# Kernel optimization log

Hardware: AMD Instinct MI355X
Metric: run time of the kernel (lower is better)

The kernel has to match this reference:

```python
import jax, jax.numpy as jnp
import numpy as np
import math

TWO_PI = 2.0 * math.pi
LN_EPS = 1e-5


def _phase(pos_f, d):
    # periods[i, j] = i * d + j + 2 ; phi[s, i, j] = cos(2*pi*k_s / periods[i, j])
    i = jnp.arange(d, dtype=jnp.float32)
    periods = i[:, None] * d + i[None, :] + 2.0  # (d, d)
    return jnp.cos(TWO_PI * pos_f[:, None, None] / periods)  # (S, d, d)


def _layernorm(x, g, b):
    mu = jnp.mean(x, axis=-1, keepdims=True)
    var = jnp.mean(jnp.square(x - mu), axis=-1, keepdims=True)
    return (x - mu) * jax.lax.rsqrt(var + LN_EPS) * g + b


def _pos_nk(x, P, phi):
    # Nk[b, s, i] = sum_j P[i, j] * x[b, s, j] * phi[s, i, j]
    return jnp.einsum('bsj,ij,sij->bsi', x, P, phi)


def setup_inputs() -> dict:
    key = jax.random.key(0)
    ks = jax.random.split(key, 10)
    B, S, V, D = 4, 4096, 64, 128
    NTOK = 64  # 4^3 k-mer tokens
    u = lambda k, shp, a: jax.random.uniform(k, shp, jnp.float32, -a, a)
    return {
        'tokens': jax.random.randint(ks[0], (B, S), 0, NTOK, dtype=jnp.int32),
        'positions': jnp.arange(S, dtype=jnp.int32),
        'emb': jax.random.normal(ks[1], (NTOK, V), jnp.float32),
        'char_P': u(ks[2], (V, V), 0.1),
        'M1': u(ks[3], (D, V), 0.5),
        'P1': u(ks[4], (D, D), 0.1),
        'g1': jnp.ones((D,), jnp.float32),
        'b1': jnp.zeros((D,), jnp.float32),
        'R1': u(ks[5], (D, V), 0.1),
        'M2': u(ks[6], (D, D), 0.5),
        'P2': u(ks[7], (D, D), 0.1),
        'g2': jnp.ones((D,), jnp.float32),
        'b2': jnp.zeros((D,), jnp.float32),
    }


def reference(tokens, positions, emb, char_P, M1, P1, g1, b1, R1, M2, P2, g2, b2):
    pos_f = positions.astype(jnp.float32)
    V, D1, D2 = emb.shape[1], M1.shape[0], M2.shape[0]
    # char level (Layer 0): embedding + position-modulated mixing
    x = emb[tokens]                               # (B, S, V)
    h = _pos_nk(x, char_P, _phase(pos_f, V))      # (B, S, V)
    # Layer 1: separate residual (in_dim != out_dim -> linear proj)
    t1 = jnp.einsum('bsj,ij->bsi', h, M1)         # (B, S, D1)
    n1 = _pos_nk(_layernorm(t1, g1, b1), P1, _phase(pos_f, D1))
    h1 = n1 + jnp.einsum('bsj,ij->bsi', h, R1)
    # Layer 2: shared residual (residual = x @ M.T, pre-norm)
    t2 = jnp.einsum('bsj,ij->bsi', h1, M2)        # (B, S, D2)
    n2 = _pos_nk(_layernorm(t2, g2, b2), P2, _phase(pos_f, D2))
    return n2 + t2
```

## Files before the change

kernel.cpp:

```cpp
#include <hip/hip_runtime.h>

typedef unsigned short u16;
typedef unsigned int   u32;
typedef float f32x2 __attribute__((ext_vector_type(2)));

#define BB 4
#define SS 4096
#define VV 64
#define DD 128

#define CPT_OFF 0
#define M1T_OFF 4096
#define R1T_OFF 12288
#define P1T_OFF 20480
#define M2T_OFF 36864
#define P2T_OFF 53248
#define EMB_OFF 69632
#define G1_OFF  73728
#define B1_OFF  73856
#define G2_OFF  73984
#define B2_OFF  74112
#define WS_F32_WEIGHTS 74240

__device__ __forceinline__ float bf2f(u16 u) {
    return __uint_as_float(((u32)u) << 16);
}
__device__ __forceinline__ float ldany(const void* p, int idx, bool f32) {
    return f32 ? ((const float*)p)[idx] : bf2f(((const u16*)p)[idx]);
}
__device__ __forceinline__ float phase_cos(float pos, float pf) {
    float x = pos * __builtin_amdgcn_rcpf(pf);
    float r = __builtin_amdgcn_fractf(x);
    return __builtin_amdgcn_cosf(r);
}
__device__ __forceinline__ float f4get(float4 v, int i) {
    return i == 0 ? v.x : i == 1 ? v.y : i == 2 ? v.z : v.w;
}
struct acc2x2 {
    f32x2 lo, hi;
    __device__ __forceinline__ void zero() { lo = (f32x2)0.f; hi = (f32x2)0.f; }
    __device__ __forceinline__ void fma(float s, float4 v) {
        f32x2 s2 = {s, s};
        f32x2 vlo = {v.x, v.y}, vhi = {v.z, v.w};
        lo = __builtin_elementwise_fma(s2, vlo, lo);
        hi = __builtin_elementwise_fma(s2, vhi, hi);
    }
    __device__ __forceinline__ float get(int b) const {
        return b == 0 ? lo[0] : b == 1 ? lo[1] : b == 2 ? hi[0] : hi[1];
    }
    __device__ __forceinline__ void red_xor(int m) {
        lo[0] += __shfl_xor(lo[0], m, 64);
        lo[1] += __shfl_xor(lo[1], m, 64);
        hi[0] += __shfl_xor(hi[0], m, 64);
        hi[1] += __shfl_xor(hi[1], m, 64);
    }
};

__global__ void prep_ws(const void* __restrict__ cP,  const void* __restrict__ M1,
                        const void* __restrict__ R1,  const void* __restrict__ P1,
                        const void* __restrict__ M2,  const void* __restrict__ P2,
                        const void* __restrict__ emb, const void* __restrict__ g1,
                        const void* __restrict__ b1,  const void* __restrict__ g2,
                        const void* __restrict__ b2,  float* __restrict__ wsf)
{
    const bool f32 = (((const u32*)g1)[0] == 0x3F800000u);
    const int m = blockIdx.x;
    const int t = threadIdx.x;
    if (m == 17) {
        for (int idx = t; idx < 4608; idx += 256) {
            float v; int dst;
            if (idx < 4096) { v = ldany(emb, idx, f32); dst = EMB_OFF + idx; }
            else {
                int off = idx - 4096, which = off >> 7, e = off & 127;
                const void* p = (which == 0) ? g1 : (which == 1) ? b1
                              : (which == 2) ? g2 : b2;
                v = ldany(p, e, f32);
                dst = G1_OFF + which * 128 + e;
            }
            wsf[dst] = v;
        }
        return;
    }
    __shared__ float tile[64][65];
    const void* src; int doff, R, C, ti0, tj0;
    if (m == 0)      { src = cP; doff = CPT_OFF; R = 64;  C = 64;  ti0 = 0;            tj0 = 0; }
    else if (m <= 2) { src = M1; doff = M1T_OFF; R = 128; C = 64;  ti0 = (m - 1) * 64; tj0 = 0; }
    else if (m <= 4) { src = R1; doff = R1T_OFF; R = 128; C = 64;  ti0 = (m - 3) * 64; tj0 = 0; }
    else {
        const int k = m - 5, w = k >> 2, q = k & 3;
        src  = (w == 0) ? P1 : (w == 1) ? M2 : P2;
        doff = (w == 0) ? P1T_OFF : (w == 1) ? M2T_OFF : P2T_OFF;
        R = 128; C = 128; ti0 = (q >> 1) * 64; tj0 = (q & 1) * 64;
    }
    float* dst = wsf + doff;
    #pragma unroll
    for (int k = 0; k < 16; ++k) {
        int idx = k * 256 + t;
        int i = idx >> 6, j = idx & 63;
        tile[i][j] = ldany(src, (ti0 + i) * C + (tj0 + j), f32);
    }
    __syncthreads();
    #pragma unroll
    for (int k = 0; k < 16; ++k) {
        int idx = k * 256 + t;
        int j = idx >> 6, i = idx & 63;
        int gj = tj0 + j, gi = ti0 + i;
        dst[((gj >> 2) * R + gi) * 4 + (gj & 3)] = tile[i][j];
    }
}

template<bool WS>
__global__ void __launch_bounds__(256, 3)
fused_hier(const int* __restrict__ tokens,
           const int* __restrict__ positions,
           const void* __restrict__ emb,
           const void* __restrict__ cP,
           const void* __restrict__ M1,
           const void* __restrict__ P1,
           const void* __restrict__ g1,
           const void* __restrict__ b1,
           const void* __restrict__ R1,
           const void* __restrict__ M2,
           const void* __restrict__ P2,
           const void* __restrict__ g2,
           const void* __restrict__ b2,
           const float* __restrict__ wsf,
           float* __restrict__ out)
{
    __shared__ float4 x4v[67];
    __shared__ float4 h4v[VV];
    __shared__ float4 lnv[131];
    __shared__ float4 h1v[131];
    __shared__ float  t14p[4 * DD];
    __shared__ float  t2p[4 * DD];
    __shared__ float  resp[4 * DD];

    float* x4  = (float*)x4v;
    float* h4  = (float*)h4v;
    float* lnf = (float*)lnv;
    float* h1f = (float*)h1v;

    const int t = threadIdx.x;
    const int s = blockIdx.x;
    if (s >= SS) return;
    const bool f32 = WS ? true : (((const u32*)g1)[0] == 0x3F800000u);
    const float pos = (float)positions[s];
    const int wv = t >> 6, L = t & 63;
    const int rp = wv * 16 + (L & 15);
    const int jq = (L >> 4) & 3;
    const int i7 = wv * 32 + (L & 31);
    const int jh = L >> 5;
    const int w  = wv, l = L;

    {
        int tok = tokens[wv * SS + s];
        int ie  = t & 63;
        float v = WS ? wsf[EMB_OFF + tok * VV + ie] : ldany(emb, tok * VV + ie, f32);
        x4[(ie + (ie >> 4)) * 4 + wv] = v;
    }
    __syncthreads();

    {
        acc2x2 a; a.zero();
        const int jb = jq * 16;
        float pf = (float)(rp * VV + jb + 2);
        #pragma unroll
        for (int q = 0; q < 4; ++q) {
            const int jg = jq * 4 + q;
            float4 w4;
            if (WS) w4 = *(const float4*)&wsf[CPT_OFF + (jg * VV + rp) * 4];
            #pragma unroll
            for (int k = 0; k < 4; ++k) {
                const int j = jb + q * 4 + k;
                float c  = phase_cos(pos, pf);
                float wt = (WS ? f4get(w4, k) : ldany(cP, rp * VV + j, f32)) * c;
                a.fma(wt, x4v[j + (j >> 4)]);
                pf += 1.0f;
            }
        }
        a.red_xor(16);
        a.red_xor(32);
        h4[rp * 4 + jq] = a.get(jq);
    }
    __syncthreads();

    {
        acc2x2 at, ar; at.zero(); ar.zero();
        #pragma unroll
        for (int q = 0; q < 8; ++q) {
            const int jg = jh * 8 + q;
            float4 m4, r4;
            if (WS) {
                m4 = *(const float4*)&wsf[M1T_OFF + (jg * DD + i7) * 4];
                r4 = *(const float4*)&wsf[R1T_OFF + (jg * DD + i7) * 4];
            }
            #pragma unroll
            for (int k = 0; k < 4; ++k) {
                const int j = jh * 32 + q * 4 + k;
                float mv = WS ? f4get(m4, k) : ldany(M1, i7 * VV + j, f32);
                float rv = WS ? f4get(r4, k) : ldany(R1, i7 * VV + j, f32);
                float4 hb = h4v[j];
                at.fma(mv, hb);
                ar.fma(rv, hb);
            }
        }
        at.red_xor(32);
        ar.red_xor(32);
        const int b0 = jh * 2, b1 = b0 + 1;
        t14p[b0 * 128 + i7] = at.get(b0);
        t14p[b1 * 128 + i7] = at.get(b1);
        resp[b0 * 128 + i7] = ar.get(b0);
        resp[b1 * 128 + i7] = ar.get(b1);
    }
    __syncthreads();

    {
        float v0 = t14p[w * 128 + l], v1 = t14p[w * 128 + 64 + l];
        float s1 = v0 + v1;
        #pragma unroll
        for (int m = 1; m < 64; m <<= 1) s1 += __shfl_xor(s1, m, 64);
        float mu = s1 * (1.0f / 128.0f);
        float d0 = v0 - mu, d1 = v1 - mu;
        float s2 = d0 * d0 + d1 * d1;
        #pragma unroll
        for (int m = 1; m < 64; m <<= 1) s2 += __shfl_xor(s2, m, 64);
        float rs = rsqrtf(s2 * (1.0f / 128.0f) + 1e-5f);
        float ga = WS ? wsf[G1_OFF + l]      : ldany(g1, l, f32);
        float gb = WS ? wsf[G1_OFF + l + 64] : ldany(g1, l + 64, f32);
        float ba = WS ? wsf[B1_OFF + l]      : ldany(b1, l, f32);
        float bb = WS ? wsf[B1_OFF + l + 64] : ldany(b1, l + 64, f32);
        const int pA = l + (l >> 5);
        const int pB = l + 66 + (l >> 5);
        lnf[pA * 4 + w] = d0 * rs * ga + ba;
        lnf[pB * 4 + w] = d1 * rs * gb + bb;
    }
    __syncthreads();

    {
        acc2x2 alo, ahi; alo.zero(); ahi.zero();
        const int jb = jq * 32;
        float pfa = (float)(rp * DD + jb + 2);
        float pfb = pfa + 8192.0f;
        #pragma unroll
        for (int q = 0; q < 8; ++q) {
            const int jg = jq * 8 + q;
            float4 wa, wb;
            if (WS) {
                wa = *(const float4*)&wsf[P1T_OFF + (jg * DD + rp) * 4];
                wb = *(const float4*)&wsf[P1T_OFF + (jg * DD + rp + 64) * 4];
            }
            #pragma unroll
            for (int k = 0; k < 4; ++k) {
                const int j = jb + q * 4 + k;
                float ca = phase_cos(pos, pfa);
                float cb = phase_cos(pos, pfb);
                float4 lnj = lnv[j + (j >> 5)];
                float wva = WS ? f4get(wa, k) : ldany(P1, rp * DD + j, f32);
                float wvb = WS ? f4get(wb, k) : ldany(P1, (rp + 64) * DD + j, f32);
                alo.fma(wva * ca, lnj);
                ahi.fma(wvb * cb, lnj);
                pfa += 1.0f; pfb += 1.0f;
            }
        }
        alo.red_xor(16); alo.red_xor(32);
        ahi.red_xor(16); ahi.red_xor(32);
        float r0 = resp[jq * 128 + rp];
        float r1 = resp[jq * 128 + rp + 64];
        h1f[(rp + (rp >> 5)) * 4 + jq]      = r0 + alo.get(jq);
        h1f[(rp + 66 + (rp >> 5)) * 4 + jq] = r1 + ahi.get(jq);
    }
    __syncthreads();

    float t2v0, t2v1;
    {
        acc2x2 alo, ahi; alo.zero(); ahi.zero();
        const int jb = jq * 32;
        #pragma unroll
        for (int q = 0; q < 8; ++q) {
            const int jg = jq * 8 + q;
            float4 wa, wb;
            if (WS) {
                wa = *(const float4*)&wsf[M2T_OFF + (jg * DD + rp) * 4];
                wb = *(const float4*)&wsf[M2T_OFF + (jg * DD + rp + 64) * 4];
            }
            #pragma unroll
            for (int k = 0; k < 4; ++k) {
                const int j = jb + q * 4 + k;
                float4 hj = h1v[j + (j >> 5)];
                float wva = WS ? f4get(wa, k) : ldany(M2, rp * DD + j, f32);
                float wvb = WS ? f4get(wb, k) : ldany(M2, (rp + 64) * DD + j, f32);
                alo.fma(wva, hj);
                ahi.fma(wvb, hj);
            }
        }
        alo.red_xor(16); alo.red_xor(32);
        ahi.red_xor(16); ahi.red_xor(32);
        t2v0 = alo.get(jq);
        t2v1 = ahi.get(jq);
        t2p[jq * 128 + rp]      = t2v0;
        t2p[jq * 128 + rp + 64] = t2v1;
    }
    __syncthreads();

    {
        float v0 = t2p[w * 128 + l], v1 = t2p[w * 128 + 64 + l];
        float s1 = v0 + v1;
        #pragma unroll
        for (int m = 1; m < 64; m <<= 1) s1 += __shfl_xor(s1, m, 64);
        float mu = s1 * (1.0f / 128.0f);
        float d0 = v0 - mu, d1 = v1 - mu;
        float s2 = d0 * d0 + d1 * d1;
        #pragma unroll
        for (int m = 1; m < 64; m <<= 1) s2 += __shfl_xor(s2, m, 64);
        float rs = rsqrtf(s2 * (1.0f / 128.0f) + 1e-5f);
        float ga = WS ? wsf[G2_OFF + l]      : ldany(g2, l, f32);
        float gb = WS ? wsf[G2_OFF + l + 64] : ldany(g2, l + 64, f32);
        float ba = WS ? wsf[B2_OFF + l]      : ldany(b2, l, f32);
        float bb = WS ? wsf[B2_OFF + l + 64] : ldany(b2, l + 64, f32);
        const int pA = l + (l >> 5);
        const int pB = l + 66 + (l >> 5);
        lnf[pA * 4 + w] = d0 * rs * ga + ba;
        lnf[pB * 4 + w] = d1 * rs * gb + bb;
    }
    __syncthreads();

    {
        acc2x2 alo, ahi; alo.zero(); ahi.zero();
        const int jb = jq * 32;
        float pfa = (float)(rp * DD + jb + 2);
        float pfb = pfa + 8192.0f;
        #pragma unroll
        for (int q = 0; q < 8; ++q) {
            const int jg = jq * 8 + q;
            float4 wa, wb;
            if (WS) {
                wa = *(const float4*)&wsf[P2T_OFF + (jg * DD + rp) * 4];
                wb = *(const float4*)&wsf[P2T_OFF + (jg * DD + rp + 64) * 4];
            }
            #pragma unroll
            for (int k = 0; k < 4; ++k) {
                const int j = jb + q * 4 + k;
                float ca = phase_cos(pos, pfa);
                float cb = phase_cos(pos, pfb);
                float4 lnj = lnv[j + (j >> 5)];
                float wva = WS ? f4get(wa, k) : ldany(P2, rp * DD + j, f32);
                float wvb = WS ? f4get(wb, k) : ldany(P2, (rp + 64) * DD + j, f32);
                alo.fma(wva * ca, lnj);
                ahi.fma(wvb * cb, lnj);
                pfa += 1.0f; pfb += 1.0f;
            }
        }
        alo.red_xor(16); alo.red_xor(32);
        ahi.red_xor(16); ahi.red_xor(32);
        out[(jq * SS + s) * DD + rp]      = alo.get(jq) + t2v0;
        out[(jq * SS + s) * DD + rp + 64] = ahi.get(jq) + t2v1;
    }
}

extern "C" void kernel_launch(void* const* d_in, const int* in_sizes, int n_in,
                              void* d_out, int out_size, void* d_ws, size_t ws_size,
                              hipStream_t stream)
{
    const int* tokens    = (const int*)d_in[0];
    const int* positions = (const int*)d_in[1];
    const void* emb = d_in[2];
    const void* cP  = d_in[3];
    const void* M1  = d_in[4];
    const void* P1  = d_in[5];
    const void* g1  = d_in[6];
    const void* b1  = d_in[7];
    const void* R1  = d_in[8];
    const void* M2  = d_in[9];
    const void* P2  = d_in[10];
    const void* g2  = d_in[11];
    const void* b2  = d_in[12];
    float* out = (float*)d_out;
    float* wsf = (float*)d_ws;

    const bool tw = (ws_size >= (size_t)WS_F32_WEIGHTS * sizeof(float));
    if (tw) {
        prep_ws<<<18, 256, 0, stream>>>(cP, M1, R1, P1, M2, P2, emb,
                                        g1, b1, g2, b2, wsf);
        fused_hier<true><<<SS, 256, 0, stream>>>(tokens, positions, emb, cP, M1, P1,
                                                 g1, b1, R1, M2, P2, g2, b2, wsf, out);
    } else {
        fused_hier<false><<<SS, 256, 0, stream>>>(tokens, positions, emb, cP, M1, P1,
                                                  g1, b1, R1, M2, P2, g2, b2, wsf, out);
    }
}
```

Before: 154.7 us.

## Use one wavefront per position with full reductions per lane

Each position's block shrinks from four wavefronts to one 64-lane wavefront. Every lane now owns whole output rows and runs the full reduction dimension itself, which removes the cross-lane shuffle reductions after each matvec. Each lane also computes all four batch LayerNorms in one pass. The trade-off is four times the serial work per thread, including the cosine phase evaluations, and fewer threads per block, so the kernel depends on many concurrent blocks to hide latency.

Measured after the change: 164.7 us. 1.06x slower.

```diff
diff --git a/kernel.cpp b/kernel.cpp
--- a/kernel.cpp
+++ b/kernel.cpp
@@ -22,6 +22,8 @@
 #define B2_OFF  74112
 #define WS_F32_WEIGHTS 74240
 
+#define SK(j) ((j) + ((j) >> 3))
+
 __device__ __forceinline__ float bf2f(u16 u) {
     return __uint_as_float(((u32)u) << 16);
 }
@@ -48,11 +50,8 @@
     __device__ __forceinline__ float get(int b) const {
         return b == 0 ? lo[0] : b == 1 ? lo[1] : b == 2 ? hi[0] : hi[1];
     }
-    __device__ __forceinline__ void red_xor(int m) {
-        lo[0] += __shfl_xor(lo[0], m, 64);
-        lo[1] += __shfl_xor(lo[1], m, 64);
-        hi[0] += __shfl_xor(hi[0], m, 64);
-        hi[1] += __shfl_xor(hi[1], m, 64);
+    __device__ __forceinline__ float4 as4() const {
+        return make_float4(lo[0], lo[1], hi[0], hi[1]);
     }
 };
 
@@ -110,7 +109,7 @@
 }
 
 template<bool WS>
-__global__ void __launch_bounds__(256, 3)
+__global__ void __launch_bounds__(64, 3)
 fused_hier(const int* __restrict__ tokens,
            const int* __restrict__ positions,
            const void* __restrict__ emb,
@@ -127,233 +126,259 @@
            const float* __restrict__ wsf,
            float* __restrict__ out)
 {
-    __shared__ float4 x4v[67];
-    __shared__ float4 h4v[VV];
-    __shared__ float4 lnv[131];
-    __shared__ float4 h1v[131];
-    __shared__ float  t14p[4 * DD];
-    __shared__ float  t2p[4 * DD];
-    __shared__ float  resp[4 * DD];
-
-    float* x4  = (float*)x4v;
-    float* h4  = (float*)h4v;
-    float* lnf = (float*)lnv;
-    float* h1f = (float*)h1v;
-
-    const int t = threadIdx.x;
+    __shared__ float4 x4v[72];
+    __shared__ float4 h4v[72];
+    __shared__ float4 lnv[144];
+    __shared__ float4 h1v[144];
+    __shared__ float  t14p[512];
+    __shared__ float  t2p[512];
+
+    const int l = threadIdx.x;
     const int s = blockIdx.x;
     if (s >= SS) return;
     const bool f32 = WS ? true : (((const u32*)g1)[0] == 0x3F800000u);
     const float pos = (float)positions[s];
-    const int wv = t >> 6, L = t & 63;
-    const int rp = wv * 16 + (L & 15);
-    const int jq = (L >> 4) & 3;
-    const int i7 = wv * 32 + (L & 31);
-    const int jh = L >> 5;
-    const int w  = wv, l = L;
-
-    {
-        int tok = tokens[wv * SS + s];
-        int ie  = t & 63;
-        float v = WS ? wsf[EMB_OFF + tok * VV + ie] : ldany(emb, tok * VV + ie, f32);
-        x4[(ie + (ie >> 4)) * 4 + wv] = v;
+
+    {
+        int tk0 = tokens[0 * SS + s], tk1 = tokens[1 * SS + s];
+        int tk2 = tokens[2 * SS + s], tk3 = tokens[3 * SS + s];
+        float4 xb;
+        xb.x = WS ? wsf[EMB_OFF + tk0 * VV + l] : ldany(emb, tk0 * VV + l, f32);
+        xb.y = WS ? wsf[EMB_OFF + tk1 * VV + l] : ldany(emb, tk1 * VV + l, f32);
+        xb.z = WS ? wsf[EMB_OFF + tk2 * VV + l] : ldany(emb, tk2 * VV + l, f32);
+        xb.w = WS ? wsf[EMB_OFF + tk3 * VV + l] : ldany(emb, tk3 * VV + l, f32);
+        x4v[SK(l)] = xb;
     }
     __syncthreads();
 
     {
         acc2x2 a; a.zero();
-        const int jb = jq * 16;
-        float pf = (float)(rp * VV + jb + 2);
-        #pragma unroll
-        for (int q = 0; q < 4; ++q) {
-            const int jg = jq * 4 + q;
+        float pf = (float)(l * VV + 2);
+        #pragma unroll
+        for (int q = 0; q < 16; ++q) {
             float4 w4;
-            if (WS) w4 = *(const float4*)&wsf[CPT_OFF + (jg * VV + rp) * 4];
+            if (WS) w4 = *(const float4*)&wsf[CPT_OFF + (q * VV + l) * 4];
             #pragma unroll
             for (int k = 0; k < 4; ++k) {
-                const int j = jb + q * 4 + k;
+                const int j = q * 4 + k;
                 float c  = phase_cos(pos, pf);
-                float wt = (WS ? f4get(w4, k) : ldany(cP, rp * VV + j, f32)) * c;
-                a.fma(wt, x4v[j + (j >> 4)]);
+                float wt = (WS ? f4get(w4, k) : ldany(cP, l * VV + j, f32)) * c;
+                a.fma(wt, x4v[SK(j)]);
                 pf += 1.0f;
             }
         }
-        a.red_xor(16);
-        a.red_xor(32);
-        h4[rp * 4 + jq] = a.get(jq);
-    }
-    __syncthreads();
-
-    {
-        acc2x2 at, ar; at.zero(); ar.zero();
-        #pragma unroll
-        for (int q = 0; q < 8; ++q) {
-            const int jg = jh * 8 + q;
-            float4 m4, r4;
+        h4v[SK(l)] = a.as4();
+    }
+    __syncthreads();
+
+    float4 res0, res1;
+    {
+        acc2x2 at0, at1, ar0, ar1;
+        at0.zero(); at1.zero(); ar0.zero(); ar1.zero();
+        #pragma unroll 8
+        for (int q = 0; q < 16; ++q) {
+            float4 ma, mb, ra, rb;
             if (WS) {
-                m4 = *(const float4*)&wsf[M1T_OFF + (jg * DD + i7) * 4];
-                r4 = *(const float4*)&wsf[R1T_OFF + (jg * DD + i7) * 4];
+                ma = *(const float4*)&wsf[M1T_OFF + (q * DD + l) * 4];
+                mb = *(const float4*)&wsf[M1T_OFF + (q * DD + l + 64) * 4];
+                ra = *(const float4*)&wsf[R1T_OFF + (q * DD + l) * 4];
+                rb = *(const float4*)&wsf[R1T_OFF + (q * DD + l + 64) * 4];
             }
             #pragma unroll
             for (int k = 0; k < 4; ++k) {
-                const int j = jh * 32 + q * 4 + k;
-                float mv = WS ? f4get(m4, k) : ldany(M1, i7 * VV + j, f32);
-                float rv = WS ? f4get(r4, k) : ldany(R1, i7 * VV + j, f32);
-                float4 hb = h4v[j];
-                at.fma(mv, hb);
-                ar.fma(rv, hb);
-            }
-        }
-        at.red_xor(32);
-        ar.red_xor(32);
-        const int b0 = jh * 2, b1 = b0 + 1;
-        t14p[b0 * 128 + i7] = at.get(b0);
-        t14p[b1 * 128 + i7] = at.get(b1);
-        resp[b0 * 128 + i7] = ar.get(b0);
-        resp[b1 * 128 + i7] = ar.get(b1);
-    }
-    __syncthreads();
-
-    {
-        float v0 = t14p[w * 128 + l], v1 = t14p[w * 128 + 64 + l];
-        float s1 = v0 + v1;
-        #pragma unroll
-        for (int m = 1; m < 64; m <<= 1) s1 += __shfl_xor(s1, m, 64);
-        float mu = s1 * (1.0f / 128.0f);
-        float d0 = v0 - mu, d1 = v1 - mu;
-        float s2 = d0 * d0 + d1 * d1;
-        #pragma unroll
-        for (int m = 1; m < 64; m <<= 1) s2 += __shfl_xor(s2, m, 64);
-        float rs = rsqrtf(s2 * (1.0f / 128.0f) + 1e-5f);
+                const int j = q * 4 + k;
+                float4 hb = h4v[SK(j)];
+                float m0 = WS ? f4get(ma, k) : ldany(M1, l * VV + j, f32);
+                float m1 = WS ? f4get(mb, k) : ldany(M1, (l + 64) * VV + j, f32);
+                float r0 = WS ? f4get(ra, k) : ldany(R1, l * VV + j, f32);
+                float r1 = WS ? f4get(rb, k) : ldany(R1, (l + 64) * VV + j, f32);
+                at0.fma(m0, hb); at1.fma(m1, hb);
+                ar0.fma(r0, hb); ar1.fma(r1, hb);
+            }
+        }
+        #pragma unroll
+        for (int b = 0; b < 4; ++b) {
+            t14p[b * 128 + l]      = at0.get(b);
+            t14p[b * 128 + l + 64] = at1.get(b);
+        }
+        res0 = ar0.as4();
+        res1 = ar1.as4();
+    }
+    __syncthreads();
+
+    {
+        float v0[4], v1[4], sm[4];
+        #pragma unroll
+        for (int b = 0; b < 4; ++b) {
+            v0[b] = t14p[b * 128 + l];
+            v1[b] = t14p[b * 128 + l + 64];
+            sm[b] = v0[b] + v1[b];
+        }
+        #pragma unroll
+        for (int m = 1; m < 64; m <<= 1) {
+            #pragma unroll
+            for (int b = 0; b < 4; ++b) sm[b] += __shfl_xor(sm[b], m, 64);
+        }
+        float va[4];
+        #pragma unroll
+        for (int b = 0; b < 4; ++b) {
+            float mu = sm[b] * (1.0f / 128.0f);
+            v0[b] -= mu; v1[b] -= mu;
+            va[b] = v0[b] * v0[b] + v1[b] * v1[b];
+        }
+        #pragma unroll
+        for (int m = 1; m < 64; m <<= 1) {
+            #pragma unroll
+            for (int b = 0; b < 4; ++b) va[b] += __shfl_xor(va[b], m, 64);
+        }
         float ga = WS ? wsf[G1_OFF + l]      : ldany(g1, l, f32);
         float gb = WS ? wsf[G1_OFF + l + 64] : ldany(g1, l + 64, f32);
         float ba = WS ? wsf[B1_OFF + l]      : ldany(b1, l, f32);
         float bb = WS ? wsf[B1_OFF + l + 64] : ldany(b1, l + 64, f32);
-        const int pA = l + (l >> 5);
-        const int pB = l + 66 + (l >> 5);
-        lnf[pA * 4 + w] = d0 * rs * ga + ba;
-        lnf[pB * 4 + w] = d1 * rs * gb + bb;
+        float4 lo, hi;
+        #pragma unroll
+        for (int b = 0; b < 4; ++b) {
+            float rs = rsqrtf(va[b] * (1.0f / 128.0f) + 1e-5f);
+            ((float*)&lo)[b] = v0[b] * rs * ga + ba;
+            ((float*)&hi)[b] = v1[b] * rs * gb + bb;
+        }
+        lnv[SK(l)]      = lo;
+        lnv[SK(l + 64)] = hi;
     }
     __syncthreads();
 
     {
         acc2x2 alo, ahi; alo.zero(); ahi.zero();
-        const int jb = jq * 32;
-        float pfa = (float)(rp * DD + jb + 2);
+        float pfa = (float)(l * DD + 2);
         float pfb = pfa + 8192.0f;
-        #pragma unroll
-        for (int q = 0; q < 8; ++q) {
-            const int jg = jq * 8 + q;
+        #pragma unroll 8
+        for (int q = 0; q < 32; ++q) {
             float4 wa, wb;
             if (WS) {
-                wa = *(const float4*)&wsf[P1T_OFF + (jg * DD + rp) * 4];
-                wb = *(const float4*)&wsf[P1T_OFF + (jg * DD + rp + 64) * 4];
+                wa = *(const float4*)&wsf[P1T_OFF + (q * DD + l) * 4];
+                wb = *(const float4*)&wsf[P1T_OFF + (q * DD + l + 64) * 4];
             }
             #pragma unroll
             for (int k = 0; k < 4; ++k) {
-                const int j = jb + q * 4 + k;
+                const int j = q * 4 + k;
                 float ca = phase_cos(pos, pfa);
                 float cb = phase_cos(pos, pfb);
-                float4 lnj = lnv[j + (j >> 5)];
-                float wva = WS ? f4get(wa, k) : ldany(P1, rp * DD + j, f32);
-                float wvb = WS ? f4get(wb, k) : ldany(P1, (rp + 64) * DD + j, f32);
-                alo.fma(wva * ca, lnj);
-                ahi.fma(wvb * cb, lnj);
+                float4 lnj = lnv[SK(j)];
+                float w0 = WS ? f4get(wa, k) : ldany(P1, l * DD + j, f32);
+                float w1 = WS ? f4get(wb, k) : ldany(P1, (l + 64) * DD + j, f32);
+                alo.fma(w0 * ca, lnj);
+                ahi.fma(w1 * cb, lnj);
                 pfa += 1.0f; pfb += 1.0f;
             }
         }
-        alo.red_xor(16); alo.red_xor(32);
-        ahi.red_xor(16); ahi.red_xor(32);
-        float r0 = resp[jq * 128 + rp];
-        float r1 = resp[jq * 128 + rp + 64];
-        h1f[(rp + (rp >> 5)) * 4 + jq]      = r0 + alo.get(jq);
-        h1f[(rp + 66 + (rp >> 5)) * 4 + jq] = r1 + ahi.get(jq);
-    }
-    __syncthreads();
-
-    float t2v0, t2v1;
+        float4 h1lo = alo.as4(), h1hi = ahi.as4();
+        h1v[SK(l)]      = make_float4(h1lo.x + res0.x, h1lo.y + res0.y,
+                                      h1lo.z + res0.z, h1lo.w + res0.w);
+        h1v[SK(l + 64)] = make_float4(h1hi.x + res1.x, h1hi.y + res1.y,
+                                      h1hi.z + res1.z, h1hi.w + res1.w);
+    }
+    __syncthreads();
+
+    float4 t2a, t2b;
     {
         acc2x2 alo, ahi; alo.zero(); ahi.zero();
-        const int jb = jq * 32;
-        #pragma unroll
-        for (int q = 0; q < 8; ++q) {
-            const int jg = jq * 8 + q;
+        #pragma unroll 8
+        for (int q = 0; q < 32; ++q) {
             float4 wa, wb;
             if (WS) {
-                wa = *(const float4*)&wsf[M2T_OFF + (jg * DD + rp) * 4];
-                wb = *(const float4*)&wsf[M2T_OFF + (jg * DD + rp + 64) * 4];
+                wa = *(const float4*)&wsf[M2T_OFF + (q * DD + l) * 4];
+                wb = *(const float4*)&wsf[M2T_OFF + (q * DD + l + 64) * 4];
             }
             #pragma unroll
             for (int k = 0; k < 4; ++k) {
-                const int j = jb + q * 4 + k;
-                float4 hj = h1v[j + (j >> 5)];
-                float wva = WS ? f4get(wa, k) : ldany(M2, rp * DD + j, f32);
-                float wvb = WS ? f4get(wb, k) : ldany(M2, (rp + 64) * DD + j, f32);
-                alo.fma(wva, hj);
-                ahi.fma(wvb, hj);
-            }
-        }
-        alo.red_xor(16); alo.red_xor(32);
-        ahi.red_xor(16); ahi.red_xor(32);
-        t2v0 = alo.get(jq);
-        t2v1 = ahi.get(jq);
-        t2p[jq * 128 + rp]      = t2v0;
-        t2p[jq * 128 + rp + 64] = t2v1;
-    }
-    __syncthreads();
-
-    {
-        float v0 = t2p[w * 128 + l], v1 = t2p[w * 128 + 64 + l];
-        float s1 = v0 + v1;
-        #pragma unroll
-        for (int m = 1; m < 64; m <<= 1) s1 += __shfl_xor(s1, m, 64);
-        float mu = s1 * (1.0f / 128.0f);
-        float d0 = v0 - mu, d1 = v1 - mu;
-        float s2 = d0 * d0 + d1 * d1;
-        #pragma unroll
-        for (int m = 1; m < 64; m <<= 1) s2 += __shfl_xor(s2, m, 64);
-        float rs = rsqrtf(s2 * (1.0f / 128.0f) + 1e-5f);
+                const int j = q * 4 + k;
+                float4 hj = h1v[SK(j)];
+                float w0 = WS ? f4get(wa, k) : ldany(M2, l * DD + j, f32);
+                float w1 = WS ? f4get(wb, k) : ldany(M2, (l + 64) * DD + j, f32);
+                alo.fma(w0, hj);
+                ahi.fma(w1, hj);
+            }
+        }
+        t2a = alo.as4();
+        t2b = ahi.as4();
+        #pragma unroll
+        for (int b = 0; b < 4; ++b) {
+            t2p[b * 128 + l]      = f4get(t2a, b);
+            t2p[b * 128 + l + 64] = f4get(t2b, b);
+        }
+    }
+    __syncthreads();
+
+    {
+        float v0[4], v1[4], sm[4];
+        #pragma unroll
+        for (int b = 0; b < 4; ++b) {
+            v0[b] = t2p[b * 128 + l];
+            v1[b] = t2p[b * 128 + l + 64];
+            sm[b] = v0[b] + v1[b];
+        }
+        #pragma unroll
+        for (int m = 1; m < 64; m <<= 1) {
+            #pragma unroll
+            for (int b = 0; b < 4; ++b) sm[b] += __shfl_xor(sm[b], m, 64);
+        }
+        float va[4];
+        #pragma unroll
+        for (int b = 0; b < 4; ++b) {
+            float mu = sm[b] * (1.0f / 128.0f);
+            v0[b] -= mu; v1[b] -= mu;
+            va[b] = v0[b] * v0[b] + v1[b] * v1[b];
+        }
+        #pragma unroll
+        for (int m = 1; m < 64; m <<= 1) {
+            #pragma unroll
+            for (int b = 0; b < 4; ++b) va[b] += __shfl_xor(va[b], m, 64);
+        }
         float ga = WS ? wsf[G2_OFF + l]      : ldany(g2, l, f32);
         float gb = WS ? wsf[G2_OFF + l + 64] : ldany(g2, l + 64, f32);
         float ba = WS ? wsf[B2_OFF + l]      : ldany(b2, l, f32);
         float bb = WS ? wsf[B2_OFF + l + 64] : ldany(b2, l + 64, f32);
-        const int pA = l + (l >> 5);
-        const int pB = l + 66 + (l >> 5);
-        lnf[pA * 4 + w] = d0 * rs * ga + ba;
-        lnf[pB * 4 + w] = d1 * rs * gb + bb;
+        float4 lo, hi;
+        #pragma unroll
+        for (int b = 0; b < 4; ++b) {
+            float rs = rsqrtf(va[b] * (1.0f / 128.0f) + 1e-5f);
+            ((float*)&lo)[b] = v0[b] * rs * ga + ba;
+            ((float*)&hi)[b] = v1[b] * rs * gb + bb;
+        }
+        lnv[SK(l)]      = lo;
+        lnv[SK(l + 64)] = hi;
     }
     __syncthreads();
 
     {
         acc2x2 alo, ahi; alo.zero(); ahi.zero();
-        const int jb = jq * 32;
-        float pfa = (float)(rp * DD + jb + 2);
+        float pfa = (float)(l * DD + 2);
         float pfb = pfa + 8192.0f;
-        #pragma unroll
-        for (int q = 0; q < 8; ++q) {
-            const int jg = jq * 8 + q;
+        #pragma unroll 8
+        for (int q = 0; q < 32; ++q) {
             float4 wa, wb;
             if (WS) {
-                wa = *(const float4*)&wsf[P2T_OFF + (jg * DD + rp) * 4];
-                wb = *(const float4*)&wsf[P2T_OFF + (jg * DD + rp + 64) * 4];
+                wa = *(const float4*)&wsf[P2T_OFF + (q * DD + l) * 4];
+                wb = *(const float4*)&wsf[P2T_OFF + (q * DD + l + 64) * 4];
             }
             #pragma unroll
             for (int k = 0; k < 4; ++k) {
-                const int j = jb + q * 4 + k;
+                const int j = q * 4 + k;
                 float ca = phase_cos(pos, pfa);
                 float cb = phase_cos(pos, pfb);
-                float4 lnj = lnv[j + (j >> 5)];
-                float wva = WS ? f4get(wa, k) : ldany(P2, rp * DD + j, f32);
-                float wvb = WS ? f4get(wb, k) : ldany(P2, (rp + 64) * DD + j, f32);
-                alo.fma(wva * ca, lnj);
-                ahi.fma(wvb * cb, lnj);
+                float4 lnj = lnv[SK(j)];
+                float w0 = WS ? f4get(wa, k) : ldany(P2, l * DD + j, f32);
+                float w1 = WS ? f4get(wb, k) : ldany(P2, (l + 64) * DD + j, f32);
+                alo.fma(w0 * ca, lnj);
+                ahi.fma(w1 * cb, lnj);
                 pfa += 1.0f; pfb += 1.0f;
             }
         }
-        alo.red_xor(16); alo.red_xor(32);
-        ahi.red_xor(16); ahi.red_xor(32);
-        out[(jq * SS + s) * DD + rp]      = alo.get(jq) + t2v0;
-        out[(jq * SS + s) * DD + rp + 64] = ahi.get(jq) + t2v1;
+        #pragma unroll
+        for (int b = 0; b < 4; ++b) {
+            out[(b * SS + s) * DD + l]      = alo.get(b) + f4get(t2a, b);
+            out[(b * SS + s) * DD + l + 64] = ahi.get(b) + f4get(t2b, b);
+        }
     }
 }
 
@@ -381,10 +406,10 @@
     if (tw) {
         prep_ws<<<18, 256, 0, stream>>>(cP, M1, R1, P1, M2, P2, emb,
                                         g1, b1, g2, b2, wsf);
-        fused_hier<true><<<SS, 256, 0, stream>>>(tokens, positions, emb, cP, M1, P1,
+        fused_hier<true><<<SS, 64, 0, stream>>>(tokens, positions, emb, cP, M1, P1,
+                                                g1, b1, R1, M2, P2, g2, b2, wsf, out);
+    } else {
+        fused_hier<false><<<SS, 64, 0, stream>>>(tokens, positions, emb, cP, M1, P1,
                                                  g1, b1, R1, M2, P2, g2, b2, wsf, out);
-    } else {
-        fused_hier<false><<<SS, 256, 0, stream>>>(tokens, positions, emb, cP, M1, P1,
-                                                  g1, b1, R1, M2, P2, g2, b2, wsf, out);
-    }
-}
+    }
+}
```
